# Kernel tuning notes

Measured on AMD Instinct MI355X. Metric: run time of the kernel, lower is better.

## Reference

```python
import jax, jax.numpy as jnp
import numpy as np

N_NODES = 100000
N_EDGES = 3200000
N_GRAPHS = 64
HEADS = 8
NEG_SLOPE = 0.2


def gat_conv(x, W, a_src, a_dst, b, src, dst, heads, out_ch):
    """PyG GATConv (concat=True, add_self_loops=True, negative_slope=0.2, eval mode).
    x: [N, F_in]; W: [F_in, heads*out_ch]; a_src/a_dst: [heads, out_ch]; b: [heads*out_ch].
    src/dst already include self loops. Softmax over edges sharing a dst node.
    """
    n = x.shape[0]
    h = (x @ W).reshape(n, heads, out_ch)            # [N, H, C]
    alpha_src = jnp.einsum('nhc,hc->nh', h, a_src)   # [N, H]
    alpha_dst = jnp.einsum('nhc,hc->nh', h, a_dst)   # [N, H]
    e = jax.nn.leaky_relu(alpha_src[src] + alpha_dst[dst], NEG_SLOPE)  # [E, H]
    m = jax.ops.segment_max(e, dst, num_segments=n)
    e = jnp.exp(e - m[dst])
    denom = jax.ops.segment_sum(e, dst, num_segments=n)
    alpha = e / (denom[dst] + 1e-16)                 # [E, H]
    msg = alpha[:, :, None] * h[src]                 # [E, H, C]
    out = jax.ops.segment_sum(msg, dst, num_segments=n)  # [N, H, C]
    return out.reshape(n, heads * out_ch) + b


def setup_inputs() -> dict:
    key = jax.random.key(0)
    ks = jax.random.split(key, 24)
    x = jax.random.normal(ks[0], (N_NODES, 128), dtype=jnp.float32)
    edge_index = jax.random.randint(ks[1], (2, N_EDGES), 0, N_NODES, dtype=jnp.int32)
    batch = jnp.sort(jax.random.randint(ks[2], (N_NODES,), 0, N_GRAPHS, dtype=jnp.int32))

    def glorot(k, shape):
        fan_in, fan_out = shape[0], shape[-1]
        lim = np.sqrt(6.0 / (fan_in + fan_out)).astype(np.float32)
        return jax.random.uniform(k, shape, jnp.float32, -lim, lim)

    params = {
        'W1': glorot(ks[3], (128, 64)),
        'a_src1': glorot(ks[4], (HEADS, 8)),
        'a_dst1': glorot(ks[5], (HEADS, 8)),
        'b1': jnp.zeros((64,), jnp.float32),
        'W2': glorot(ks[6], (64, 128)),
        'a_src2': glorot(ks[7], (HEADS, 16)),
        'a_dst2': glorot(ks[8], (HEADS, 16)),
        'b2': jnp.zeros((128,), jnp.float32),
        'fc1_w': glorot(ks[9], (128, 256)),  'fc1_b': jnp.zeros((256,), jnp.float32),
        'fc2_w': glorot(ks[10], (256, 512)), 'fc2_b': jnp.zeros((512,), jnp.float32),
        'fc3_w': glorot(ks[11], (512, 512)), 'fc3_b': jnp.zeros((512,), jnp.float32),
        'fc4_w': glorot(ks[12], (512, 100)), 'fc4_b': jnp.zeros((100,), jnp.float32),
    }
    return {'x': x, 'edge_index': edge_index, 'batch': batch, **params}


def reference(x, edge_index, batch,
              W1, a_src1, a_dst1, b1,
              W2, a_src2, a_dst2, b2,
              fc1_w, fc1_b, fc2_w, fc2_b, fc3_w, fc3_b, fc4_w, fc4_b):
    n = x.shape[0]
    loop = jnp.arange(n, dtype=edge_index.dtype)
    src = jnp.concatenate([edge_index[0], loop])
    dst = jnp.concatenate([edge_index[1], loop])

    h = gat_conv(x, W1, a_src1, a_dst1, b1, src, dst, HEADS, 8)
    h = jax.nn.relu(h)
    h = gat_conv(h, W2, a_src2, a_dst2, b2, src, dst, HEADS, 16)
    h = jax.nn.relu(h)

    # global_mean_pool over batch ids
    sums = jax.ops.segment_sum(h, batch, num_segments=N_GRAPHS)        # [G, 128]
    counts = jax.ops.segment_sum(jnp.ones((n,), h.dtype), batch, num_segments=N_GRAPHS)
    g = sums / jnp.maximum(counts, 1.0)[:, None]

    g = jax.nn.relu(g @ fc1_w + fc1_b)
    g = jax.nn.relu(g @ fc2_w + fc2_b)
    g = jax.nn.relu(g @ fc3_w + fc3_b)
    g = g @ fc4_w + fc4_b
    return g.reshape(-1, 10, 10)
```

## Files before the change

kernel.cpp:

```cpp
#include <hip/hip_runtime.h>
#include <hip/hip_bf16.h>

#define NN 100000
#define NE 3200000
#define ET (NE + NN)
#define NG 64
#define BINBITS 10
#define NBINS 98
#define EPB 16
#define LOG2E 1.44269504088896f

__device__ __forceinline__ unsigned bfr(float x) {
  unsigned u = __float_as_uint(x);
  return (u + 0x7FFFu + ((u >> 16) & 1u)) >> 16;
}

__device__ __forceinline__ unsigned fkey(float x) {
  unsigned b = __float_as_uint(x);
  return (b & 0x80000000u) ? ~b : (b | 0x80000000u);
}

__device__ __forceinline__ float gmax_decode(unsigned k) {
  return __uint_as_float((k & 0x80000000u) ? (k & 0x7FFFFFFFu) : ~k);
}

__global__ void init_counts_k(int* counts) {
  int i = blockIdx.x * 256 + threadIdx.x;
  if (i < NN) counts[i] = 1;
}

__global__ void count_k(const int* __restrict__ dst, int* __restrict__ counts) {
  int i = blockIdx.x * 256 + threadIdx.x;
  if (i < NE) atomicAdd(&counts[dst[i]], 1);
}

__global__ __launch_bounds__(1024) void scan1_k(const int* __restrict__ cnt, int* __restrict__ csum) {
  __shared__ int lds[1024];
  int i = blockIdx.x * 1024 + threadIdx.x;
  lds[threadIdx.x] = (i < NN) ? cnt[i] : 0;
  __syncthreads();
  for (int off = 512; off > 0; off >>= 1) {
    if (threadIdx.x < off) lds[threadIdx.x] += lds[threadIdx.x + off];
    __syncthreads();
  }
  if (threadIdx.x == 0) csum[blockIdx.x] = lds[0];
}

__global__ __launch_bounds__(128) void scan2_k(int* csum, int nch) {
  __shared__ int lds[128];
  int v = (threadIdx.x < nch) ? csum[threadIdx.x] : 0;
  lds[threadIdx.x] = v;
  __syncthreads();
  for (int off = 1; off < 128; off <<= 1) {
    int t = (threadIdx.x >= off) ? lds[threadIdx.x - off] : 0;
    __syncthreads();
    lds[threadIdx.x] += t;
    __syncthreads();
  }
  if (threadIdx.x < nch) csum[threadIdx.x] = lds[threadIdx.x] - v;
}

__global__ __launch_bounds__(1024) void scan3_k(const int* __restrict__ cnt, const int* __restrict__ csum,
                                                int* __restrict__ indptr, int* __restrict__ cursor) {
  __shared__ int lds[1024];
  int i = blockIdx.x * 1024 + threadIdx.x;
  int v = (i < NN) ? cnt[i] : 0;
  lds[threadIdx.x] = v;
  __syncthreads();
  for (int off = 1; off < 1024; off <<= 1) {
    int t = (threadIdx.x >= off) ? lds[threadIdx.x - off] : 0;
    __syncthreads();
    lds[threadIdx.x] += t;
    __syncthreads();
  }
  int excl = csum[blockIdx.x] + lds[threadIdx.x] - v;
  if (i < NN) { indptr[i] = excl; cursor[i] = excl; }
  else if (i == NN) indptr[NN] = ET;
}

__global__ void bininit_k(const int* __restrict__ indptr, int* __restrict__ binbase, int* __restrict__ bincur) {
  int b = threadIdx.x;
  if (b <= NBINS) {
    int node = b << BINBITS; if (node > NN) node = NN;
    int v = indptr[node];
    binbase[b] = v;
    if (b < NBINS) bincur[b] = v;
  }
}

__global__ __launch_bounds__(256) void binA_k(const int* __restrict__ ei, int* __restrict__ bincur,
                                              unsigned* __restrict__ binbuf) {
  __shared__ int lhist[NBINS], lbase[NBINS];
  int t = threadIdx.x;
  for (int i = t; i < NBINS; i += 256) lhist[i] = 0;
  __syncthreads();
  long base = (long)blockIdx.x * (256 * EPB);
  unsigned pk[EPB]; int bn[EPB];
  #pragma unroll
  for (int j = 0; j < EPB; j++) {
    long i = base + j * 256 + t;
    if (i < ET) {
      int s, d;
      if (i < NE) { s = ei[i]; d = ei[NE + i]; }
      else { s = (int)(i - NE); d = s; }
      int b = d >> BINBITS;
      bn[j] = b;
      pk[j] = ((unsigned)s << BINBITS) | (unsigned)(d & 1023);
      atomicAdd(&lhist[b], 1);
    } else bn[j] = -1;
  }
  __syncthreads();
  for (int i = t; i < NBINS; i += 256) {
    int c = lhist[i];
    lbase[i] = c ? atomicAdd(&bincur[i], c) : 0;
    lhist[i] = 0;
  }
  __syncthreads();
  #pragma unroll
  for (int j = 0; j < EPB; j++) {
    if (bn[j] >= 0) {
      int off = atomicAdd(&lhist[bn[j]], 1);
      binbuf[lbase[bn[j]] + off] = pk[j];
    }
  }
}

#define SEGS 8
__global__ __launch_bounds__(256) void binB_k(const unsigned* __restrict__ binbuf, const int* __restrict__ binbase,
                                              int* __restrict__ cursor, int* __restrict__ srcs) {
  int r = blockIdx.x & 7;
  int m = blockIdx.x >> 3;
  int q = m / SEGS, seg = m % SEGS;
  int bin = q * 8 + r;
  if (bin >= NBINS) return;
  int b0 = binbase[bin], b1 = binbase[bin + 1];
  int n = b1 - b0;
  int per = (n + SEGS - 1) / SEGS;
  int e0 = b0 + seg * per;
  int e1 = min(e0 + per, b1);
  int dbase = bin << BINBITS;
  for (int i = e0 + threadIdx.x; i < e1; i += 256) {
    unsigned p = binbuf[i];
    int d = dbase | (int)(p & 1023u);
    int s = (int)(p >> BINBITS);
    int slot = atomicAdd(&cursor[d], 1);
    srcs[slot] = s;
  }
}

__global__ __launch_bounds__(256) void gemm1_k(const float* __restrict__ x, const float* __restrict__ W,
                                               const float* __restrict__ a_s, const float* __restrict__ a_d,
                                               unsigned* __restrict__ h1bf, float* __restrict__ asrc,
                                               float* __restrict__ adst, unsigned* __restrict__ gmaxg) {
  __shared__ float ldsW[128 * 64];
  __shared__ unsigned gm8[8];
  int t = threadIdx.x;
  int n0 = blockIdx.x * 64;
  if (t < 8) gm8[t] = 0;
  {
    const float4* W4 = (const float4*)W;
    float4* lw = (float4*)ldsW;
    #pragma unroll
    for (int r = 0; r < 8; r++) lw[r * 256 + t] = W4[r * 256 + t];
  }
  __syncthreads();
  int cg = t & 15, ng = t >> 4;
  const float* xr0 = x + (size_t)min(n0 + ng * 4 + 0, NN - 1) * 128;
  const float* xr1 = x + (size_t)min(n0 + ng * 4 + 1, NN - 1) * 128;
  const float* xr2 = x + (size_t)min(n0 + ng * 4 + 2, NN - 1) * 128;
  const float* xr3 = x + (size_t)min(n0 + ng * 4 + 3, NN - 1) * 128;
  float acc[4][4] = {};
  #pragma unroll 4
  for (int k = 0; k < 128; k += 2) {
    float2 xv0 = *(const float2*)&xr0[k];
    float2 xv1 = *(const float2*)&xr1[k];
    float2 xv2 = *(const float2*)&xr2[k];
    float2 xv3 = *(const float2*)&xr3[k];
    float4 w0 = *(const float4*)&ldsW[k * 64 + cg * 4];
    float4 w1 = *(const float4*)&ldsW[(k + 1) * 64 + cg * 4];
    acc[0][0] += xv0.x * w0.x + xv0.y * w1.x;
    acc[0][1] += xv0.x * w0.y + xv0.y * w1.y;
    acc[0][2] += xv0.x * w0.z + xv0.y * w1.z;
    acc[0][3] += xv0.x * w0.w + xv0.y * w1.w;
    acc[1][0] += xv1.x * w0.x + xv1.y * w1.x;
    acc[1][1] += xv1.x * w0.y + xv1.y * w1.y;
    acc[1][2] += xv1.x * w0.z + xv1.y * w1.z;
    acc[1][3] += xv1.x * w0.w + xv1.y * w1.w;
    acc[2][0] += xv2.x * w0.x + xv2.y * w1.x;
    acc[2][1] += xv2.x * w0.y + xv2.y * w1.y;
    acc[2][2] += xv2.x * w0.z + xv2.y * w1.z;
    acc[2][3] += xv2.x * w0.w + xv2.y * w1.w;
    acc[3][0] += xv3.x * w0.x + xv3.y * w1.x;
    acc[3][1] += xv3.x * w0.y + xv3.y * w1.y;
    acc[3][2] += xv3.x * w0.z + xv3.y * w1.z;
    acc[3][3] += xv3.x * w0.w + xv3.y * w1.w;
  }
  int head = cg >> 1, sub = (cg & 1) * 4;
  float as0 = a_s[head * 8 + sub], as1 = a_s[head * 8 + sub + 1];
  float as2 = a_s[head * 8 + sub + 2], as3 = a_s[head * 8 + sub + 3];
  float ad0 = a_d[head * 8 + sub], ad1 = a_d[head * 8 + sub + 1];
  float ad2 = a_d[head * 8 + sub + 2], ad3 = a_d[head * 8 + sub + 3];
  #pragma unroll
  for (int i = 0; i < 4; i++) {
    float vs = acc[i][0] * as0 + acc[i][1] * as1 + acc[i][2] * as2 + acc[i][3] * as3;
    float vd = acc[i][0] * ad0 + acc[i][1] * ad1 + acc[i][2] * ad2 + acc[i][3] * ad3;
    vs += __shfl_xor(vs, 1, 64);
    vd += __shfl_xor(vd, 1, 64);
    vs *= LOG2E; vd *= LOG2E;
    int gn = n0 + ng * 4 + i;
    if (gn < NN) {
      unsigned p0 = bfr(acc[i][0]) | (bfr(acc[i][1]) << 16);
      unsigned p1 = bfr(acc[i][2]) | (bfr(acc[i][3]) << 16);
      ((uint2*)(h1bf + (size_t)gn * 32))[cg] = make_uint2(p0, p1);
      if ((cg & 1) == 0) {
        asrc[gn * 8 + head] = vs;
        adst[gn * 8 + head] = vd;
        atomicMax(&gm8[head], fkey(vs));
      }
    }
  }
  __syncthreads();
  if (t < 8) atomicMax(&gmaxg[t], gm8[t]);
}

__global__ __launch_bounds__(256) void agg1_k(const unsigned* __restrict__ h1bf, const float* __restrict__ asrc,
                                              const float* __restrict__ adst_, const int* __restrict__ indptr,
                                              const int* __restrict__ srcs, const float* __restrict__ b,
                                              const unsigned* __restrict__ gmax, float* __restrict__ z1) {
  int wave = threadIdx.x >> 6, lane = threadIdx.x & 63;
  int node = blockIdx.x * 4 + wave;
  int s0 = indptr[node], s1 = indptr[node + 1];
  int grp = lane >> 4, q = lane & 15;
  int head = q >> 1;
  float ad = adst_[node * 8 + head];
  float ub = gmax_decode(gmax[head]) + ad; ub = fmaxf(ub, 0.2f * ub);
  const uint2* hp = (const uint2*)h1bf;
  float d = 0.f, a0 = 0.f, a1 = 0.f, a2 = 0.f, a3 = 0.f;
  for (int base = s0; base < s1; base += 64) {
    int i = base + lane;
    int sv = (i < s1) ? srcs[i] : 0;
    int n = s1 - base; if (n > 64) n = 64;
    for (int j = 0; j < n; j += 4) {
      int jj = j + grp;
      int s = __shfl(sv, jj, 64);
      float e = asrc[s * 8 + head] + ad;
      e = fmaxf(e, 0.2f * e);
      float w = __builtin_amdgcn_exp2f(e - ub);
      if (jj >= n) w = 0.f;
      uint2 u = hp[(size_t)s * 16 + q];
      d += w;
      a0 += w * __uint_as_float(u.x << 16);
      a1 += w * __uint_as_float(u.x & 0xFFFF0000u);
      a2 += w * __uint_as_float(u.y << 16);
      a3 += w * __uint_as_float(u.y & 0xFFFF0000u);
    }
  }
  d  += __shfl_xor(d, 16, 64);  d  += __shfl_xor(d, 32, 64);
  a0 += __shfl_xor(a0, 16, 64); a0 += __shfl_xor(a0, 32, 64);
  a1 += __shfl_xor(a1, 16, 64); a1 += __shfl_xor(a1, 32, 64);
  a2 += __shfl_xor(a2, 16, 64); a2 += __shfl_xor(a2, 32, 64);
  a3 += __shfl_xor(a3, 16, 64); a3 += __shfl_xor(a3, 32, 64);
  if (grp == 0) {
    float inv = 1.f / (d + 1e-16f);
    float o0 = a0 * inv + b[4 * q];
    float o1 = a1 * inv + b[4 * q + 1];
    float o2 = a2 * inv + b[4 * q + 2];
    float o3 = a3 * inv + b[4 * q + 3];
    float4 ov;
    ov.x = o0 > 0.f ? o0 : 0.f;
    ov.y = o1 > 0.f ? o1 : 0.f;
    ov.z = o2 > 0.f ? o2 : 0.f;
    ov.w = o3 > 0.f ? o3 : 0.f;
    ((float4*)z1)[node * 16 + q] = ov;
  }
}

__global__ __launch_bounds__(256) void gemm2_k(const float* __restrict__ z1, const float* __restrict__ W,
                                               const float* __restrict__ a_s, const float* __restrict__ a_d,
                                               uint2* __restrict__ h2bf, float* __restrict__ asrc,
                                               float* __restrict__ adst, unsigned* __restrict__ gmaxg) {
  __shared__ float ldsW[64 * 128];
  __shared__ unsigned gm8[8];
  int t = threadIdx.x;
  int n0 = blockIdx.x * 64;
  if (t < 8) gm8[t] = 0;
  {
    const float4* W4 = (const float4*)W;
    float4* lw = (float4*)ldsW;
    #pragma unroll
    for (int r = 0; r < 8; r++) lw[r * 256 + t] = W4[r * 256 + t];
  }
  __syncthreads();
  int cg = t & 15, ng = t >> 4;
  int c0 = cg * 8;
  const float* zr0 = z1 + (size_t)min(n0 + ng * 4 + 0, NN - 1) * 64;
  const float* zr1 = z1 + (size_t)min(n0 + ng * 4 + 1, NN - 1) * 64;
  const float* zr2 = z1 + (size_t)min(n0 + ng * 4 + 2, NN - 1) * 64;
  const float* zr3 = z1 + (size_t)min(n0 + ng * 4 + 3, NN - 1) * 64;
  float acc[4][8] = {};
  #pragma unroll 2
  for (int k = 0; k < 64; k += 2) {
    float2 xv[4];
    xv[0] = *(const float2*)&zr0[k];
    xv[1] = *(const float2*)&zr1[k];
    xv[2] = *(const float2*)&zr2[k];
    xv[3] = *(const float2*)&zr3[k];
    float4 wa0 = *(const float4*)&ldsW[k * 128 + c0];
    float4 wa1 = *(const float4*)&ldsW[k * 128 + c0 + 4];
    float4 wb0 = *(const float4*)&ldsW[(k + 1) * 128 + c0];
    float4 wb1 = *(const float4*)&ldsW[(k + 1) * 128 + c0 + 4];
    #pragma unroll
    for (int i = 0; i < 4; i++) {
      acc[i][0] += xv[i].x * wa0.x + xv[i].y * wb0.x;
      acc[i][1] += xv[i].x * wa0.y + xv[i].y * wb0.y;
      acc[i][2] += xv[i].x * wa0.z + xv[i].y * wb0.z;
      acc[i][3] += xv[i].x * wa0.w + xv[i].y * wb0.w;
      acc[i][4] += xv[i].x * wa1.x + xv[i].y * wb1.x;
      acc[i][5] += xv[i].x * wa1.y + xv[i].y * wb1.y;
      acc[i][6] += xv[i].x * wa1.z + xv[i].y * wb1.z;
      acc[i][7] += xv[i].x * wa1.w + xv[i].y * wb1.w;
    }
  }
  int head = cg >> 1, sub = (cg & 1) * 8;
  float asv[8], adv[8];
  #pragma unroll
  for (int j = 0; j < 8; j++) {
    asv[j] = a_s[head * 16 + sub + j];
    adv[j] = a_d[head * 16 + sub + j];
  }
  #pragma unroll
  for (int i = 0; i < 4; i++) {
    float vs = 0.f, vd = 0.f;
    #pragma unroll
    for (int j = 0; j < 8; j++) { vs += acc[i][j] * asv[j]; vd += acc[i][j] * adv[j]; }
    vs += __shfl_xor(vs, 1, 64);
    vd += __shfl_xor(vd, 1, 64);
    vs *= LOG2E; vd *= LOG2E;
    int gn = n0 + ng * 4 + i;
    if (gn < NN) {
      unsigned p0 = bfr(acc[i][0]) | (bfr(acc[i][1]) << 16);
      unsigned p1 = bfr(acc[i][2]) | (bfr(acc[i][3]) << 16);
      unsigned p2 = bfr(acc[i][4]) | (bfr(acc[i][5]) << 16);
      unsigned p3 = bfr(acc[i][6]) | (bfr(acc[i][7]) << 16);
      ((uint4*)h2bf)[(size_t)gn * 16 + cg] = make_uint4(p0, p1, p2, p3);
      if ((cg & 1) == 0) {
        asrc[gn * 8 + head] = vs;
        adst[gn * 8 + head] = vd;
        atomicMax(&gm8[head], fkey(vs));
      }
    }
  }
  __syncthreads();
  if (t < 8) atomicMax(&gmaxg[t], gm8[t]);
}

__global__ __launch_bounds__(256) void agg2_k(const uint2* __restrict__ h2bf, const float* __restrict__ asrc,
                                              const float* __restrict__ adst_, const int* __restrict__ indptr,
                                              const int* __restrict__ srcs, const float* __restrict__ b,
                                              const unsigned* __restrict__ gmax, float* __restrict__ z2) {
  int wave = threadIdx.x >> 6, lane = threadIdx.x & 63;
  int node = blockIdx.x * 4 + wave;
  int s0 = indptr[node], s1 = indptr[node + 1];
  int grp = lane >> 4, q = lane & 15;
  int head = q >> 1;
  float ad = adst_[node * 8 + head];
  float ub = gmax_decode(gmax[head]) + ad; ub = fmaxf(ub, 0.2f * ub);
  const uint4* hp = (const uint4*)h2bf;
  float d = 0.f;
  float a0 = 0.f, a1 = 0.f, a2 = 0.f, a3 = 0.f, a4 = 0.f, a5 = 0.f, a6 = 0.f, a7 = 0.f;
  for (int base = s0; base < s1; base += 64) {
    int i = base + lane;
    int sv = (i < s1) ? srcs[i] : 0;
    int n = s1 - base; if (n > 64) n = 64;
    for (int j = 0; j < n; j += 4) {
      int jj = j + grp;
      int s = __shfl(sv, jj, 64);
      float e = asrc[s * 8 + head] + ad;
      e = fmaxf(e, 0.2f * e);
      float w = __builtin_amdgcn_exp2f(e - ub);
      if (jj >= n) w = 0.f;
      uint4 u = hp[(size_t)s * 16 + q];
      d += w;
      a0 += w * __uint_as_float(u.x << 16);
      a1 += w * __uint_as_float(u.x & 0xFFFF0000u);
      a2 += w * __uint_as_float(u.y << 16);
      a3 += w * __uint_as_float(u.y & 0xFFFF0000u);
      a4 += w * __uint_as_float(u.z << 16);
      a5 += w * __uint_as_float(u.z & 0xFFFF0000u);
      a6 += w * __uint_as_float(u.w << 16);
      a7 += w * __uint_as_float(u.w & 0xFFFF0000u);
    }
  }
  d  += __shfl_xor(d, 16, 64);  d  += __shfl_xor(d, 32, 64);
  a0 += __shfl_xor(a0, 16, 64); a0 += __shfl_xor(a0, 32, 64);
  a1 += __shfl_xor(a1, 16, 64); a1 += __shfl_xor(a1, 32, 64);
  a2 += __shfl_xor(a2, 16, 64); a2 += __shfl_xor(a2, 32, 64);
  a3 += __shfl_xor(a3, 16, 64); a3 += __shfl_xor(a3, 32, 64);
  a4 += __shfl_xor(a4, 16, 64); a4 += __shfl_xor(a4, 32, 64);
  a5 += __shfl_xor(a5, 16, 64); a5 += __shfl_xor(a5, 32, 64);
  a6 += __shfl_xor(a6, 16, 64); a6 += __shfl_xor(a6, 32, 64);
  a7 += __shfl_xor(a7, 16, 64); a7 += __shfl_xor(a7, 32, 64);
  if (grp == 0) {
    float inv = 1.f / (d + 1e-16f);
    float o0 = a0 * inv + b[8 * q];
    float o1 = a1 * inv + b[8 * q + 1];
    float o2 = a2 * inv + b[8 * q + 2];
    float o3 = a3 * inv + b[8 * q + 3];
    float o4 = a4 * inv + b[8 * q + 4];
    float o5 = a5 * inv + b[8 * q + 5];
    float o6 = a6 * inv + b[8 * q + 6];
    float o7 = a7 * inv + b[8 * q + 7];
    float4 v0, v1;
    v0.x = o0 > 0.f ? o0 : 0.f;
    v0.y = o1 > 0.f ? o1 : 0.f;
    v0.z = o2 > 0.f ? o2 : 0.f;
    v0.w = o3 > 0.f ? o3 : 0.f;
    v1.x = o4 > 0.f ? o4 : 0.f;
    v1.y = o5 > 0.f ? o5 : 0.f;
    v1.z = o6 > 0.f ? o6 : 0.f;
    v1.w = o7 > 0.f ? o7 : 0.f;
    ((float4*)z2)[node * 32 + 2 * q] = v0;
    ((float4*)z2)[node * 32 + 2 * q + 1] = v1;
  }
}

#define POOL_NODES 512
__global__ __launch_bounds__(128) void pool_k(const float* __restrict__ h, const int* __restrict__ batch,
                                              float* __restrict__ sums, float* __restrict__ cnts) {
  int ch = threadIdx.x;
  int base = blockIdx.x * POOL_NODES;
  int end = min(base + POOL_NODES, NN);
  float acc = 0.f; int cnt = 0; int cur = batch[base];
  for (int i = base; i < end; i++) {
    int g = batch[i];
    if (g != cur) {
      atomicAdd(&sums[cur * 128 + ch], acc);
      if (ch == 0) atomicAdd(&cnts[cur], (float)cnt);
      acc = 0.f; cnt = 0; cur = g;
    }
    acc += h[(size_t)i * 128 + ch];
    cnt++;
  }
  atomicAdd(&sums[cur * 128 + ch], acc);
  if (ch == 0) atomicAdd(&cnts[cur], (float)cnt);
}

__global__ __launch_bounds__(256) void mlpfused_k(const float* __restrict__ sums, const float* __restrict__ cnts,
                                                  const float* __restrict__ w1, const float* __restrict__ bb1,
                                                  const float* __restrict__ w2, const float* __restrict__ bb2,
                                                  const float* __restrict__ w3, const float* __restrict__ bb3,
                                                  const float* __restrict__ w4, const float* __restrict__ bb4,
                                                  float* __restrict__ out) {
  __shared__ float bufA[512], bufB[512];
  int g = blockIdx.x, t = threadIdx.x;
  float inv = 1.f / fmaxf(cnts[g], 1.f);
  if (t < 128) bufA[t] = sums[g * 128 + t] * inv;
  __syncthreads();
  {
    float acc = bb1[t];
    #pragma unroll 4
    for (int k = 0; k < 128; k++) acc += bufA[k] * w1[k * 256 + t];
    bufB[t] = fmaxf(acc, 0.f);
  }
  __syncthreads();
  {
    float a0 = bb2[t], a1 = bb2[t + 256];
    #pragma unroll 4
    for (int k = 0; k < 256; k++) {
      float av = bufB[k];
      a0 += av * w2[k * 512 + t];
      a1 += av * w2[k * 512 + t + 256];
    }
    bufA[t] = fmaxf(a0, 0.f);
    bufA[t + 256] = fmaxf(a1, 0.f);
  }
  __syncthreads();
  {
    float a0 = bb3[t], a1 = bb3[t + 256];
    #pragma unroll 4
    for (int k = 0; k < 512; k++) {
      float av = bufA[k];
      a0 += av * w3[k * 512 + t];
      a1 += av * w3[k * 512 + t + 256];
    }
    bufB[t] = fmaxf(a0, 0.f);
    bufB[t + 256] = fmaxf(a1, 0.f);
  }
  __syncthreads();
  if (t < 100) {
    float acc = bb4[t];
    #pragma unroll 4
    for (int k = 0; k < 512; k++) acc += bufB[k] * w4[k * 100 + t];
    out[g * 100 + t] = acc;
  }
}

extern "C" void kernel_launch(void* const* d_in, const int* in_sizes, int n_in,
                              void* d_out, int out_size, void* d_ws, size_t ws_size,
                              hipStream_t stream) {
  const float* x      = (const float*)d_in[0];
  const int*   ei     = (const int*)d_in[1];
  const int*   batch  = (const int*)d_in[2];
  const float* W1     = (const float*)d_in[3];
  const float* a_src1 = (const float*)d_in[4];
  const float* a_dst1 = (const float*)d_in[5];
  const float* b1     = (const float*)d_in[6];
  const float* W2     = (const float*)d_in[7];
  const float* a_src2 = (const float*)d_in[8];
  const float* a_dst2 = (const float*)d_in[9];
  const float* b2     = (const float*)d_in[10];
  const float* fc1_w  = (const float*)d_in[11];
  const float* fc1_b  = (const float*)d_in[12];
  const float* fc2_w  = (const float*)d_in[13];
  const float* fc2_b  = (const float*)d_in[14];
  const float* fc3_w  = (const float*)d_in[15];
  const float* fc3_b  = (const float*)d_in[16];
  const float* fc4_w  = (const float*)d_in[17];
  const float* fc4_b  = (const float*)d_in[18];
  float* outp = (float*)d_out;

  float* z2   = (float*)d_ws;
  uint2* h2bf = (uint2*)(z2 + (size_t)NN * 128);
  float* asrc = (float*)(h2bf + (size_t)NN * 32);
  float* adst = asrc + (size_t)NN * 8;
  int* srcs   = (int*)(adst + (size_t)NN * 8);
  int* indptr = srcs + ET;
  float* sums = (float*)(indptr + NN + 1);
  float* gcnt = sums + NG * 128;
  unsigned* gmax = (unsigned*)(gcnt + NG);
  int* binbase = (int*)(gmax + 8);
  int* bincur  = binbase + NBINS + 1;
  unsigned* binbuf = (unsigned*)z2;
  int* counts = (int*)z2 + ET;
  int* cursor = counts + NN;
  unsigned* h1bf = (unsigned*)z2;
  float* z1 = z2 + (size_t)NN * 32;

  const int NCH = (NN + 1023) / 1024;

  init_counts_k<<<(NN + 255) / 256, 256, 0, stream>>>(counts);
  count_k<<<(NE + 255) / 256, 256, 0, stream>>>(ei + NE, counts);
  scan1_k<<<NCH, 1024, 0, stream>>>(counts, srcs);
  scan2_k<<<1, 128, 0, stream>>>(srcs, NCH);
  scan3_k<<<NCH, 1024, 0, stream>>>(counts, srcs, indptr, cursor);
  bininit_k<<<1, 128, 0, stream>>>(indptr, binbase, bincur);
  binA_k<<<(ET + 256 * EPB - 1) / (256 * EPB), 256, 0, stream>>>(ei, bincur, binbuf);
  {
    int nq = (NBINS + 7) / 8;
    int grid = 8 * nq * SEGS;
    binB_k<<<grid, 256, 0, stream>>>(binbuf, binbase, cursor, srcs);
  }

  const int NGEMM = (NN + 63) / 64;

  hipMemsetAsync(gmax, 0, 8 * sizeof(unsigned), stream);
  gemm1_k<<<NGEMM, 256, 0, stream>>>(x, W1, a_src1, a_dst1, h1bf, asrc, adst, gmax);
  agg1_k<<<NN / 4, 256, 0, stream>>>(h1bf, asrc, adst, indptr, srcs, b1, gmax, z1);

  hipMemsetAsync(gmax, 0, 8 * sizeof(unsigned), stream);
  gemm2_k<<<NGEMM, 256, 0, stream>>>(z1, W2, a_src2, a_dst2, h2bf, asrc, adst, gmax);
  agg2_k<<<NN / 4, 256, 0, stream>>>(h2bf, asrc, adst, indptr, srcs, b2, gmax, z2);

  hipMemsetAsync(sums, 0, (NG * 128 + NG) * sizeof(float), stream);
  pool_k<<<(NN + POOL_NODES - 1) / POOL_NODES, 128, 0, stream>>>(z2, batch, sums, gcnt);
  mlpfused_k<<<NG, 256, 0, stream>>>(sums, gcnt, fc1_w, fc1_b, fc2_w, fc2_b,
                                     fc3_w, fc3_b, fc4_w, fc4_b, outp);

  (void)in_sizes; (void)n_in; (void)out_size; (void)ws_size;
}
```

Baseline: 852.2 us.

## Split fused MLP into split-K tiled kernels with atomic accumulation

```diff
diff --git a/kernel.cpp b/kernel.cpp
--- a/kernel.cpp
+++ b/kernel.cpp
@@ -445,53 +445,55 @@
   if (ch == 0) atomicAdd(&cnts[cur], (float)cnt);
 }
 
-__global__ __launch_bounds__(256) void mlpfused_k(const float* __restrict__ sums, const float* __restrict__ cnts,
-                                                  const float* __restrict__ w1, const float* __restrict__ bb1,
-                                                  const float* __restrict__ w2, const float* __restrict__ bb2,
-                                                  const float* __restrict__ w3, const float* __restrict__ bb3,
-                                                  const float* __restrict__ w4, const float* __restrict__ bb4,
-                                                  float* __restrict__ out) {
-  __shared__ float bufA[512], bufB[512];
-  int g = blockIdx.x, t = threadIdx.x;
-  float inv = 1.f / fmaxf(cnts[g], 1.f);
-  if (t < 128) bufA[t] = sums[g * 128 + t] * inv;
-  __syncthreads();
-  {
-    float acc = bb1[t];
-    #pragma unroll 4
-    for (int k = 0; k < 128; k++) acc += bufA[k] * w1[k * 256 + t];
-    bufB[t] = fmaxf(acc, 0.f);
-  }
-  __syncthreads();
-  {
-    float a0 = bb2[t], a1 = bb2[t + 256];
-    #pragma unroll 4
-    for (int k = 0; k < 256; k++) {
-      float av = bufB[k];
-      a0 += av * w2[k * 512 + t];
-      a1 += av * w2[k * 512 + t + 256];
-    }
-    bufA[t] = fmaxf(a0, 0.f);
-    bufA[t + 256] = fmaxf(a1, 0.f);
-  }
-  __syncthreads();
-  {
-    float a0 = bb3[t], a1 = bb3[t + 256];
-    #pragma unroll 4
-    for (int k = 0; k < 512; k++) {
-      float av = bufA[k];
-      a0 += av * w3[k * 512 + t];
-      a1 += av * w3[k * 512 + t + 256];
-    }
-    bufB[t] = fmaxf(a0, 0.f);
-    bufB[t + 256] = fmaxf(a1, 0.f);
-  }
-  __syncthreads();
-  if (t < 100) {
-    float acc = bb4[t];
-    #pragma unroll 4
-    for (int k = 0; k < 512; k++) acc += bufB[k] * w4[k * 100 + t];
-    out[g * 100 + t] = acc;
+__global__ void pooldiv_k(const float* __restrict__ sums, const float* __restrict__ cnts, float* __restrict__ g) {
+  int i = blockIdx.x * 256 + threadIdx.x;
+  if (i < NG * 128) {
+    float c = cnts[i >> 7];
+    c = c < 1.f ? 1.f : c;
+    g[i] = sums[i] / c;
+  }
+}
+
+__global__ void biasinit_k(float* __restrict__ t1, const float* __restrict__ bb1,
+                           float* __restrict__ t2, const float* __restrict__ bb2,
+                           float* __restrict__ t3, const float* __restrict__ bb3,
+                           float* __restrict__ o, const float* __restrict__ bb4) {
+  int i = blockIdx.x * 256 + threadIdx.x;
+  if (i < NG * 256) t1[i] = bb1[i & 255];
+  if (i < NG * 512) { t2[i] = bb2[i & 511]; t3[i] = bb3[i & 511]; }
+  if (i < NG * 100) o[i] = bb4[i % 100];
+}
+
+template <int K, int OUT, bool RELU_IN>
+__global__ __launch_bounds__(256) void mlps_k(const float* __restrict__ in, const float* __restrict__ W,
+                                              float* __restrict__ out) {
+  __shared__ float As[64][65];
+  int t = threadIdx.x;
+  int c0 = blockIdx.x * 16;
+  int k0 = blockIdx.y * 64;
+  #pragma unroll
+  for (int r = 0; r < 16; r++) {
+    int flat = r * 256 + t;
+    int g = flat >> 6, k = flat & 63;
+    float v = in[g * K + k0 + k];
+    if (RELU_IN) v = fmaxf(v, 0.f);
+    As[k][g] = v;
+  }
+  __syncthreads();
+  int g = t & 63, cq = t >> 6;
+  int col = c0 + cq * 4;
+  if (col < OUT) {
+    float a0 = 0.f, a1 = 0.f, a2 = 0.f, a3 = 0.f;
+    #pragma unroll 8
+    for (int k = 0; k < 64; k++) {
+      float av = As[k][g];
+      float4 wv = *(const float4*)&W[(size_t)(k0 + k) * OUT + col];
+      a0 += av * wv.x; a1 += av * wv.y; a2 += av * wv.z; a3 += av * wv.w;
+    }
+    atomicAdd(&out[g * OUT + col], a0);
+    if (col + 1 < OUT) atomicAdd(&out[g * OUT + col + 1], a1);
+    if (col + 2 < OUT) atomicAdd(&out[g * OUT + col + 2], a2);
+    if (col + 3 < OUT) atomicAdd(&out[g * OUT + col + 3], a3);
   }
 }
 
@@ -527,7 +529,11 @@
   int* indptr = srcs + ET;
   float* sums = (float*)(indptr + NN + 1);
   float* gcnt = sums + NG * 128;
-  unsigned* gmax = (unsigned*)(gcnt + NG);
+  float* mlpin = gcnt + NG;
+  float* mlpt1 = mlpin + NG * 128;
+  float* mlpt2 = mlpt1 + NG * 256;
+  float* mlpt3 = mlpt2 + NG * 512;
+  unsigned* gmax = (unsigned*)(mlpt3 + NG * 512);
   int* binbase = (int*)(gmax + 8);
   int* bincur  = binbase + NBINS + 1;
   unsigned* binbuf = (unsigned*)z2;
@@ -563,8 +569,12 @@
 
   hipMemsetAsync(sums, 0, (NG * 128 + NG) * sizeof(float), stream);
   pool_k<<<(NN + POOL_NODES - 1) / POOL_NODES, 128, 0, stream>>>(z2, batch, sums, gcnt);
-  mlpfused_k<<<NG, 256, 0, stream>>>(sums, gcnt, fc1_w, fc1_b, fc2_w, fc2_b,
-                                     fc3_w, fc3_b, fc4_w, fc4_b, outp);
+  pooldiv_k<<<(NG * 128 + 255) / 256, 256, 0, stream>>>(sums, gcnt, mlpin);
+  biasinit_k<<<(NG * 512 + 255) / 256, 256, 0, stream>>>(mlpt1, fc1_b, mlpt2, fc2_b, mlpt3, fc3_b, outp, fc4_b);
+  mlps_k<128, 256, false><<<dim3(16, 2), 256, 0, stream>>>(mlpin, fc1_w, mlpt1);
+  mlps_k<256, 512, true><<<dim3(32, 4), 256, 0, stream>>>(mlpt1, fc2_w, mlpt2);
+  mlps_k<512, 512, true><<<dim3(32, 8), 256, 0, stream>>>(mlpt2, fc3_w, mlpt3);
+  mlps_k<512, 100, true><<<dim3(7, 8), 256, 0, stream>>>(mlpt3, fc4_w, outp);
 
   (void)in_sizes; (void)n_in; (void)out_size; (void)ws_size;
 }
```

Measured after the change: 809.0 us. 1.05x faster.
